# Kernel tuning notes

Hardware: AMD Instinct MI355X
Metric: run time of the kernel (lower is better)

The kernel has to match this reference:

```python
import jax, jax.numpy as jnp
import numpy as np

FEATURE_DIM = 256
NUM_STEPS = 3
NUM_GRAPHS = 2048
ATOMS_PER_GRAPH = 64
TOTAL_ATOMS = NUM_GRAPHS * ATOMS_PER_GRAPH


def setup_inputs() -> dict:
    key = jax.random.key(0)
    k_x, k1, k2, k3, k4 = jax.random.split(key, 5)
    H = FEATURE_DIM
    s = 1.0 / np.sqrt(H)
    x = jax.random.normal(k_x, (TOTAL_ATOMS, H), dtype=jnp.float32)
    batch = jnp.repeat(jnp.arange(NUM_GRAPHS, dtype=jnp.int64), ATOMS_PER_GRAPH)
    sizes = jnp.full((NUM_GRAPHS,), ATOMS_PER_GRAPH, dtype=jnp.int64)
    # LSTM params (PyTorch layout: gates ordered i, f, g, o)
    W_ih = jax.random.uniform(k1, (4 * H, H), jnp.float32, -s, s)
    W_hh = jax.random.uniform(k2, (4 * H, H), jnp.float32, -s, s)
    b_ih = jax.random.uniform(k3, (4 * H,), jnp.float32, -s, s)
    b_hh = jax.random.uniform(k4, (4 * H,), jnp.float32, -s, s)
    return {"x": x, "batch": batch, "sizes": sizes,
            "W_ih": W_ih, "W_hh": W_hh, "b_ih": b_ih, "b_hh": b_hh}


def _lstm_cell(u, hx, cx, W_ih, W_hh, b_ih, b_hh):
    # u: input [B,H]; (hx, cx): hidden/cell [B,H]
    gates = u @ W_ih.T + b_ih + hx @ W_hh.T + b_hh  # [B, 4H]
    i, f, g, o = jnp.split(gates, 4, axis=-1)
    i, f, o = jax.nn.sigmoid(i), jax.nn.sigmoid(f), jax.nn.sigmoid(o)
    c = f * cx + i * jnp.tanh(g)
    h = o * jnp.tanh(c)
    return h, c


def _segment_softmax(scores, seg, num_segments):
    m = jax.ops.segment_max(scores, seg, num_segments=num_segments)
    e = jnp.exp(scores - m[seg])
    s = jax.ops.segment_sum(e, seg, num_segments=num_segments)
    return e / s[seg]


def reference(x, batch, sizes, W_ih, W_hh, b_ih, b_hh):
    B = sizes.shape[0]
    H = x.shape[1]
    seg = batch.astype(jnp.int32)
    h = jnp.zeros((B, H), dtype=x.dtype)
    c = jnp.zeros((B, H), dtype=x.dtype)
    q = h
    r = h
    for _ in range(NUM_STEPS):
        # torch code feeds h both as LSTM input and hidden state
        q, c = _lstm_cell(h, h, c, W_ih, W_hh, b_ih, b_hh)
        scores = jnp.sum(x * q[seg], axis=-1)              # [total_atoms]
        attn = _segment_softmax(scores, seg, B)            # per-graph softmax
        r = jax.ops.segment_sum(x * attn[:, None], seg, num_segments=B)  # [B,H]
        h = r  # torch code overwrites the LSTM hidden with r
    return jnp.concatenate([q, r], axis=-1)  # [B, 2H]
```

## Files before the change

kernel.cpp:

```cpp
#include <hip/hip_runtime.h>
#include <math.h>

#define H 256
#define NB 2048
#define APG 64

typedef __attribute__((ext_vector_type(8))) short short8;
typedef __attribute__((ext_vector_type(4))) float f32x4;

__device__ __forceinline__ unsigned short f2bf(float f) {
    unsigned u = __float_as_uint(f);
    u += 0x7fff + ((u >> 16) & 1);
    return (unsigned short)(u >> 16);
}

__global__ void prep_kernel(const float* __restrict__ W_ih, const float* __restrict__ W_hh,
                            const float* __restrict__ b_ih, const float* __restrict__ b_hh,
                            unsigned short* __restrict__ Wr, float* __restrict__ br,
                            unsigned short* __restrict__ hbf, float* __restrict__ c) {
    int idx = blockIdx.x * 256 + threadIdx.x;
    if (idx < 1024 * 256) {
        int wr_row = idx >> 8, k = idx & 255;
        int hcol = wr_row >> 2, gate = wr_row & 3;
        int src = gate * 65536 + hcol * 256 + k;
        Wr[idx] = f2bf(W_ih[src] + W_hh[src]);
    }
    if (idx < 1024) {
        int hcol = idx >> 2, gate = idx & 3;
        br[idx] = b_ih[gate * 256 + hcol] + b_hh[gate * 256 + hcol];
    }
    hbf[idx] = 0;
    c[idx] = 0.f;
}

#define LDA 264
__global__ __launch_bounds__(256)
void gemm_lstm(const unsigned short* __restrict__ hbf, const unsigned short* __restrict__ Wr,
               const float* __restrict__ br, float* __restrict__ c,
               float* __restrict__ qdst, int qstride) {
    __shared__ unsigned short As[64 * LDA];
    __shared__ unsigned short Bs[64 * LDA];
    int t = threadIdx.x;
    int r0 = blockIdx.y * 64;
    int w0 = blockIdx.x * 64;
    int c0h = blockIdx.x * 16;

    #pragma unroll
    for (int p = 0; p < 8; ++p) {
        int id = p * 256 + t;
        int row = id >> 5, c8 = id & 31;
        *(short8*)&As[row * LDA + c8 * 8] = *(const short8*)&hbf[(r0 + row) * H + c8 * 8];
        *(short8*)&Bs[row * LDA + c8 * 8] = *(const short8*)&Wr[(w0 + row) * H + c8 * 8];
    }
    __syncthreads();

    int lane = t & 63, w = t >> 6;
    int ln = lane & 15, qd = lane >> 4;
    int m0 = w * 16;
    f32x4 acc[4] = {};
    #pragma unroll
    for (int kk = 0; kk < 8; ++kk) {
        short8 a = *(short8*)&As[(m0 + ln) * LDA + kk * 32 + qd * 8];
        #pragma unroll
        for (int t4 = 0; t4 < 4; ++t4) {
            short8 b = *(short8*)&Bs[(t4 * 16 + ln) * LDA + kk * 32 + qd * 8];
            acc[t4] = __builtin_amdgcn_mfma_f32_16x16x32_bf16(a, b, acc[t4], 0, 0, 0);
        }
    }
    __syncthreads();

    float* gl = (float*)As;
    #pragma unroll
    for (int t4 = 0; t4 < 4; ++t4)
        #pragma unroll
        for (int r = 0; r < 4; ++r)
            gl[(m0 + qd * 4 + r) * 68 + t4 * 16 + ln] = acc[t4][r];
    __syncthreads();

    #pragma unroll
    for (int p = 0; p < 4; ++p) {
        int idx = p * 256 + t;
        int row = idx >> 4, hc = idx & 15;
        float4 g4 = *(float4*)&gl[row * 68 + hc * 4];
        float4 b4 = *(const float4*)&br[(c0h + hc) * 4];
        float gi = g4.x + b4.x, gf = g4.y + b4.y, gg = g4.z + b4.z, go = g4.w + b4.w;
        float si = 1.f / (1.f + __expf(-gi));
        float sf = 1.f / (1.f + __expf(-gf));
        float so = 1.f / (1.f + __expf(-go));
        int cidx = (r0 + row) * H + c0h + hc;
        float cn = sf * c[cidx] + si * tanhf(gg);
        c[cidx] = cn;
        qdst[(r0 + row) * qstride + c0h + hc] = so * tanhf(cn);
    }
}

__global__ __launch_bounds__(256)
void attention(const float* __restrict__ x, const float* __restrict__ qsrc, int qstride,
               unsigned short* __restrict__ rbf, float* __restrict__ rf32, int rstride) {
    __shared__ float sc[64];
    __shared__ float pl[64];
    __shared__ float rpart[4][256];
    int g = blockIdx.x;
    int t = threadIdx.x;
    int lane = t & 63, w = t >> 6;
    float4 q4 = *(const float4*)&qsrc[g * qstride + lane * 4];
    const float* xg = x + (size_t)g * APG * H;
    float4 xa[16];
    #pragma unroll
    for (int i = 0; i < 16; ++i)
        xa[i] = *(const float4*)&xg[(i * 4 + w) * H + lane * 4];
    #pragma unroll
    for (int i = 0; i < 16; ++i) {
        float p = xa[i].x * q4.x + xa[i].y * q4.y + xa[i].z * q4.z + xa[i].w * q4.w;
        #pragma unroll
        for (int s = 32; s > 0; s >>= 1) p += __shfl_xor(p, s, 64);
        if (lane == 0) sc[i * 4 + w] = p;
    }
    __syncthreads();
    if (t < 64) {
        float s = sc[t];
        float m = s;
        #pragma unroll
        for (int d = 32; d > 0; d >>= 1) m = fmaxf(m, __shfl_xor(m, d, 64));
        float e = __expf(s - m);
        float sum = e;
        #pragma unroll
        for (int d = 32; d > 0; d >>= 1) sum += __shfl_xor(sum, d, 64);
        pl[t] = e / sum;
    }
    __syncthreads();
    float4 r4 = {0.f, 0.f, 0.f, 0.f};
    #pragma unroll
    for (int i = 0; i < 16; ++i) {
        float p = pl[i * 4 + w];
        r4.x += p * xa[i].x; r4.y += p * xa[i].y;
        r4.z += p * xa[i].z; r4.w += p * xa[i].w;
    }
    *(float4*)&rpart[w][lane * 4] = r4;
    __syncthreads();
    if (t < 64) {
        float4 o = {0.f, 0.f, 0.f, 0.f};
        #pragma unroll
        for (int ww = 0; ww < 4; ++ww) {
            float4 v = *(float4*)&rpart[ww][t * 4];
            o.x += v.x; o.y += v.y; o.z += v.z; o.w += v.w;
        }
        *(float4*)&rf32[g * rstride + t * 4] = o;
        unsigned short b0 = f2bf(o.x), b1 = f2bf(o.y), b2 = f2bf(o.z), b3 = f2bf(o.w);
        unsigned short* rb = &rbf[g * H + t * 4];
        rb[0] = b0; rb[1] = b1; rb[2] = b2; rb[3] = b3;
    }
}

extern "C" void kernel_launch(void* const* d_in, const int* in_sizes, int n_in,
                              void* d_out, int out_size, void* d_ws, size_t ws_size,
                              hipStream_t stream) {
    const float* x    = (const float*)d_in[0];
    const float* W_ih = (const float*)d_in[3];
    const float* W_hh = (const float*)d_in[4];
    const float* b_ih = (const float*)d_in[5];
    const float* b_hh = (const float*)d_in[6];
    float* out = (float*)d_out;

    char* ws = (char*)d_ws;
    unsigned short* Wr  = (unsigned short*)ws;
    float*          br  = (float*)(ws + 524288);
    unsigned short* hbf = (unsigned short*)(ws + 528384);
    float*          cbuf= (float*)(ws + 1576960);
    float*          qbuf= (float*)(ws + 3674112);
    float*          rbuf= (float*)(ws + 5771264);

    prep_kernel<<<2048, 256, 0, stream>>>(W_ih, W_hh, b_ih, b_hh, Wr, br, hbf, cbuf);
    for (int step = 0; step < 3; ++step) {
        float* qdst = (step == 2) ? out : qbuf;
        int    qs   = (step == 2) ? 512 : 256;
        float* rdst = (step == 2) ? out + 256 : rbuf;
        int    rs   = (step == 2) ? 512 : 256;
        gemm_lstm<<<dim3(16, 32), 256, 0, stream>>>(hbf, Wr, br, cbuf, qdst, qs);
        attention<<<2048, 256, 0, stream>>>(x, qdst, qs, hbf, rdst, rs);
    }
}
```

Measured before the change: 278.5 us.

## Skip first-step GEMM via zero hidden state and swizzle GEMM LDS tiles

Because h and c start at zero, the first LSTM step depends only on the biases, so a tiny single-block kernel computes one shared q/c row and the first full GEMM launch is dropped. The first attention pass broadcasts that c row into the cell buffer, which replaces the old zero-initialisation in the prep kernel. The GEMM now stages K in two halves in smaller XOR-swizzled shared memory instead of a padded layout, and attention skips writing the unused fp32 r for the intermediate steps. This removes one GEMM plus redundant writes, at the cost of an extra tiny launch and an additional barrier inside the GEMM.

```diff
diff --git a/kernel.cpp b/kernel.cpp
--- a/kernel.cpp
+++ b/kernel.cpp
@@ -16,67 +16,76 @@
 
 __global__ void prep_kernel(const float* __restrict__ W_ih, const float* __restrict__ W_hh,
                             const float* __restrict__ b_ih, const float* __restrict__ b_hh,
-                            unsigned short* __restrict__ Wr, float* __restrict__ br,
-                            unsigned short* __restrict__ hbf, float* __restrict__ c) {
+                            unsigned short* __restrict__ Wr, float* __restrict__ br) {
     int idx = blockIdx.x * 256 + threadIdx.x;
-    if (idx < 1024 * 256) {
-        int wr_row = idx >> 8, k = idx & 255;
-        int hcol = wr_row >> 2, gate = wr_row & 3;
-        int src = gate * 65536 + hcol * 256 + k;
-        Wr[idx] = f2bf(W_ih[src] + W_hh[src]);
+    int wr_row = idx >> 8, k = idx & 255;
+    int hcol = wr_row >> 2, gate = wr_row & 3;
+    int src = gate * 65536 + hcol * 256 + k;
+    Wr[idx] = f2bf(W_ih[src] + W_hh[src]);
+    if (idx < 1024) {
+        int hc = idx >> 2, gt = idx & 3;
+        br[idx] = b_ih[gt * 256 + hc] + b_hh[gt * 256 + hc];
     }
-    if (idx < 1024) {
-        int hcol = idx >> 2, gate = idx & 3;
-        br[idx] = b_ih[gate * 256 + hcol] + b_hh[gate * 256 + hcol];
-    }
-    hbf[idx] = 0;
-    c[idx] = 0.f;
 }
 
-#define LDA 264
+__global__ void lstm0(const float* __restrict__ br, float* __restrict__ q1,
+                      float* __restrict__ c1) {
+    int hc = threadIdx.x;
+    float gi = br[hc * 4 + 0], gg = br[hc * 4 + 2], go = br[hc * 4 + 3];
+    float si = 1.f / (1.f + __expf(-gi));
+    float so = 1.f / (1.f + __expf(-go));
+    float cn = si * tanhf(gg);
+    c1[hc] = cn;
+    q1[hc] = so * tanhf(cn);
+}
+
 __global__ __launch_bounds__(256)
 void gemm_lstm(const unsigned short* __restrict__ hbf, const unsigned short* __restrict__ Wr,
                const float* __restrict__ br, float* __restrict__ c,
                float* __restrict__ qdst, int qstride) {
-    __shared__ unsigned short As[64 * LDA];
-    __shared__ unsigned short Bs[64 * LDA];
+    __shared__ unsigned short smem[2][64 * 128];
+    unsigned short* As = smem[0];
+    unsigned short* Bs = smem[1];
     int t = threadIdx.x;
     int r0 = blockIdx.y * 64;
     int w0 = blockIdx.x * 64;
     int c0h = blockIdx.x * 16;
-
-    #pragma unroll
-    for (int p = 0; p < 8; ++p) {
-        int id = p * 256 + t;
-        int row = id >> 5, c8 = id & 31;
-        *(short8*)&As[row * LDA + c8 * 8] = *(const short8*)&hbf[(r0 + row) * H + c8 * 8];
-        *(short8*)&Bs[row * LDA + c8 * 8] = *(const short8*)&Wr[(w0 + row) * H + c8 * 8];
-    }
-    __syncthreads();
-
     int lane = t & 63, w = t >> 6;
     int ln = lane & 15, qd = lane >> 4;
     int m0 = w * 16;
     f32x4 acc[4] = {};
-    #pragma unroll
-    for (int kk = 0; kk < 8; ++kk) {
-        short8 a = *(short8*)&As[(m0 + ln) * LDA + kk * 32 + qd * 8];
+    for (int kc = 0; kc < 2; ++kc) {
         #pragma unroll
-        for (int t4 = 0; t4 < 4; ++t4) {
-            short8 b = *(short8*)&Bs[(t4 * 16 + ln) * LDA + kk * 32 + qd * 8];
-            acc[t4] = __builtin_amdgcn_mfma_f32_16x16x32_bf16(a, b, acc[t4], 0, 0, 0);
+        for (int p = 0; p < 4; ++p) {
+            int gid = p * 256 + t;
+            int row = gid >> 4, g = gid & 15;
+            int sg = g ^ (row & 15);
+            *(short8*)&As[row * 128 + sg * 8] =
+                *(const short8*)&hbf[(r0 + row) * H + kc * 128 + g * 8];
+            *(short8*)&Bs[row * 128 + sg * 8] =
+                *(const short8*)&Wr[(w0 + row) * H + kc * 128 + g * 8];
         }
+        __syncthreads();
+        #pragma unroll
+        for (int kk = 0; kk < 4; ++kk) {
+            int ga = (kk * 4 + qd) ^ ln;
+            short8 a = *(short8*)&As[(m0 + ln) * 128 + ga * 8];
+            #pragma unroll
+            for (int t4 = 0; t4 < 4; ++t4) {
+                int gb = (kk * 4 + qd) ^ ln;
+                short8 b = *(short8*)&Bs[(t4 * 16 + ln) * 128 + gb * 8];
+                acc[t4] = __builtin_amdgcn_mfma_f32_16x16x32_bf16(a, b, acc[t4], 0, 0, 0);
+            }
+        }
+        __syncthreads();
     }
-    __syncthreads();
-
-    float* gl = (float*)As;
+    float* gl = (float*)smem;
     #pragma unroll
     for (int t4 = 0; t4 < 4; ++t4)
         #pragma unroll
         for (int r = 0; r < 4; ++r)
             gl[(m0 + qd * 4 + r) * 68 + t4 * 16 + ln] = acc[t4][r];
     __syncthreads();
-
     #pragma unroll
     for (int p = 0; p < 4; ++p) {
         int idx = p * 256 + t;
@@ -96,19 +105,20 @@
 
 __global__ __launch_bounds__(256)
 void attention(const float* __restrict__ x, const float* __restrict__ qsrc, int qstride,
-               unsigned short* __restrict__ rbf, float* __restrict__ rf32, int rstride) {
+               unsigned short* __restrict__ hbf, const float* __restrict__ c1,
+               float* __restrict__ cdst, float* __restrict__ rf32, int rstride) {
     __shared__ float sc[64];
     __shared__ float pl[64];
     __shared__ float rpart[4][256];
-    int g = blockIdx.x;
-    int t = threadIdx.x;
+    int g = blockIdx.x, t = threadIdx.x;
     int lane = t & 63, w = t >> 6;
-    float4 q4 = *(const float4*)&qsrc[g * qstride + lane * 4];
     const float* xg = x + (size_t)g * APG * H;
     float4 xa[16];
     #pragma unroll
     for (int i = 0; i < 16; ++i)
         xa[i] = *(const float4*)&xg[(i * 4 + w) * H + lane * 4];
+    float4 q4 = *(const float4*)&qsrc[g * qstride + lane * 4];
+    if (c1) cdst[g * H + t] = c1[t];
     #pragma unroll
     for (int i = 0; i < 16; ++i) {
         float p = xa[i].x * q4.x + xa[i].y * q4.y + xa[i].z * q4.z + xa[i].w * q4.w;
@@ -118,12 +128,10 @@
     }
     __syncthreads();
     if (t < 64) {
-        float s = sc[t];
-        float m = s;
+        float s = sc[t], m = s;
         #pragma unroll
         for (int d = 32; d > 0; d >>= 1) m = fmaxf(m, __shfl_xor(m, d, 64));
-        float e = __expf(s - m);
-        float sum = e;
+        float e = __expf(s - m), sum = e;
         #pragma unroll
         for (int d = 32; d > 0; d >>= 1) sum += __shfl_xor(sum, d, 64);
         pl[t] = e / sum;
@@ -138,18 +146,9 @@
     }
     *(float4*)&rpart[w][lane * 4] = r4;
     __syncthreads();
-    if (t < 64) {
-        float4 o = {0.f, 0.f, 0.f, 0.f};
-        #pragma unroll
-        for (int ww = 0; ww < 4; ++ww) {
-            float4 v = *(float4*)&rpart[ww][t * 4];
-            o.x += v.x; o.y += v.y; o.z += v.z; o.w += v.w;
-        }
-        *(float4*)&rf32[g * rstride + t * 4] = o;
-        unsigned short b0 = f2bf(o.x), b1 = f2bf(o.y), b2 = f2bf(o.z), b3 = f2bf(o.w);
-        unsigned short* rb = &rbf[g * H + t * 4];
-        rb[0] = b0; rb[1] = b1; rb[2] = b2; rb[3] = b3;
-    }
+    float o = rpart[0][t] + rpart[1][t] + rpart[2][t] + rpart[3][t];
+    if (hbf)  hbf[g * H + t] = f2bf(o);
+    if (rf32) rf32[g * rstride + t] = o;
 }
 
 extern "C" void kernel_launch(void* const* d_in, const int* in_sizes, int n_in,
@@ -168,15 +167,14 @@
     unsigned short* hbf = (unsigned short*)(ws + 528384);
     float*          cbuf= (float*)(ws + 1576960);
     float*          qbuf= (float*)(ws + 3674112);
-    float*          rbuf= (float*)(ws + 5771264);
+    float*          q1  = (float*)(ws + 5771264);
+    float*          c1  = (float*)(ws + 5772288);
 
-    prep_kernel<<<2048, 256, 0, stream>>>(W_ih, W_hh, b_ih, b_hh, Wr, br, hbf, cbuf);
-    for (int step = 0; step < 3; ++step) {
-        float* qdst = (step == 2) ? out : qbuf;
-        int    qs   = (step == 2) ? 512 : 256;
-        float* rdst = (step == 2) ? out + 256 : rbuf;
-        int    rs   = (step == 2) ? 512 : 256;
-        gemm_lstm<<<dim3(16, 32), 256, 0, stream>>>(hbf, Wr, br, cbuf, qdst, qs);
-        attention<<<2048, 256, 0, stream>>>(x, qdst, qs, hbf, rdst, rs);
-    }
+    prep_kernel<<<1024, 256, 0, stream>>>(W_ih, W_hh, b_ih, b_hh, Wr, br);
+    lstm0<<<1, 256, 0, stream>>>(br, q1, c1);
+    attention<<<2048, 256, 0, stream>>>(x, q1, 0, hbf, c1, cbuf, nullptr, 0);
+    gemm_lstm<<<dim3(16, 32), 256, 0, stream>>>(hbf, Wr, br, cbuf, qbuf, 256);
+    attention<<<2048, 256, 0, stream>>>(x, qbuf, 256, hbf, nullptr, nullptr, nullptr, 0);
+    gemm_lstm<<<dim3(16, 32), 256, 0, stream>>>(hbf, Wr, br, cbuf, out, 512);
+    attention<<<2048, 256, 0, stream>>>(x, out, 512, nullptr, nullptr, nullptr, out + 256, 512);
 }
```

Result: faster. 270.4 us (-2.9%).
